# Kernel tuning notes

Hardware: AMD Instinct MI355X
Metric: run time of the kernel (lower is better)

The kernel has to match this reference:

```python
import jax, jax.numpy as jnp
import numpy as np

D_MODEL = 1024
N_HEADS = 16
HEAD_DIM = D_MODEL // N_HEADS
B, S = 2, 2048


def setup_inputs() -> dict:
    key = jax.random.key(0)
    ks = jax.random.split(key, 12)
    std = 1.0 / np.sqrt(D_MODEL)
    mk = lambda k: (jax.random.normal(k, (D_MODEL, D_MODEL), jnp.float32) * std)
    return {
        "query": jax.random.normal(ks[0], (B, S, D_MODEL), jnp.float32),
        "key": jax.random.normal(ks[1], (B, S, D_MODEL), jnp.float32),
        "value": jax.random.normal(ks[2], (B, S, D_MODEL), jnp.float32),
        "Wq": mk(ks[3]), "bq": jnp.zeros((D_MODEL,), jnp.float32),
        "Wk": mk(ks[4]), "bk": jnp.zeros((D_MODEL,), jnp.float32),
        "Wv": mk(ks[5]), "bv": jnp.zeros((D_MODEL,), jnp.float32),
        "Wo": mk(ks[6]), "bo": jnp.zeros((D_MODEL,), jnp.float32),
    }


def reference(query, key, value, Wq, bq, Wk, bk, Wv, bv, Wo, bo):
    b, s, d = query.shape
    # Linear projections (torch Linear: x @ W.T + b)
    q = query @ Wq.T + bq
    k = key @ Wk.T + bk
    v = value @ Wv.T + bv
    # [B, H, S, Dh]
    split = lambda x: x.reshape(b, -1, N_HEADS, HEAD_DIM).transpose(0, 2, 1, 3)
    qh, kh, vh = split(q), split(k), split(v)
    scores = jnp.einsum("bhqd,bhkd->bhqk", qh, kh) / jnp.sqrt(
        jnp.asarray(HEAD_DIM, qh.dtype))
    attn = jax.nn.softmax(scores, axis=-1)
    out = jnp.einsum("bhqk,bhkd->bhqd", attn, vh)
    out = out.transpose(0, 2, 1, 3).reshape(b, -1, N_HEADS * HEAD_DIM)
    return out @ Wo.T + bo
```

## Files before the change

kernel.cpp:

```cpp
#include <hip/hip_runtime.h>
#include <hip/hip_bf16.h>


typedef short bf16x8 __attribute__((ext_vector_type(8)));
typedef short bf16x4 __attribute__((ext_vector_type(4)));
typedef float f32x4  __attribute__((ext_vector_type(4)));

constexpr size_t NE = (size_t)4096 * 1024;
constexpr size_t NW = (size_t)1024 * 1024;

#if __has_builtin(__builtin_amdgcn_exp2f)
#define EXP2(x) __builtin_amdgcn_exp2f(x)
#else
#define EXP2(x) exp2f(x)
#endif

__device__ __forceinline__ short f2bf(float f) {
  __hip_bfloat16 h = __float2bfloat16(f);
  return *reinterpret_cast<short*>(&h);
}

__device__ __forceinline__ void cp16(const short* g, short* l) {
  __builtin_amdgcn_global_load_lds(
      (const __attribute__((address_space(1))) void*)g,
      (__attribute__((address_space(3))) void*)l, 16, 0, 0);
}

__device__ __forceinline__ int xcd_swz(int x, int nblk) {
  return (x & 7) * (nblk >> 3) + (x >> 3);
}

__global__ __launch_bounds__(256) void cvt_kernel(
    const float* q, const float* k, const float* v,
    const float* Wq, const float* Wk, const float* Wv, const float* Wo,
    short* qb, short* kb, short* vb,
    short* Wqb, short* Wkb, short* Wvb, short* Wob) {
  const int y = blockIdx.y;
  const float* s; short* d;
  if (y < 12) {
    const int t = y >> 2;
    const size_t off = (size_t)(y & 3) << 20;
    s = (t == 0 ? q : (t == 1 ? k : v)) + off;
    d = (t == 0 ? qb : (t == 1 ? kb : vb)) + off;
  } else {
    s = (y == 12 ? Wq : (y == 13 ? Wk : (y == 14 ? Wv : Wo)));
    d = (y == 12 ? Wqb : (y == 13 ? Wkb : (y == 14 ? Wvb : Wob)));
  }
  size_t i = (size_t)blockIdx.x * 256 + threadIdx.x;
  float4 val = ((const float4*)s)[i];
  bf16x4 o;
  o[0] = f2bf(val.x); o[1] = f2bf(val.y); o[2] = f2bf(val.z); o[3] = f2bf(val.w);
  ((bf16x4*)d)[i] = o;
}

__global__ __launch_bounds__(256) void gemm_qkv(
    const short* __restrict__ A0, const short* __restrict__ A1, const short* __restrict__ A2,
    const short* __restrict__ W0, const short* __restrict__ W1, const short* __restrict__ W2,
    const float* __restrict__ b0, const float* __restrict__ b1, const float* __restrict__ b2,
    short* __restrict__ C0, short* __restrict__ C1, short* __restrict__ Cv) {
  __shared__ short As[3][128 * 32];
  __shared__ short Bs[3][128 * 32];
  const int which = blockIdx.y;
  const short* A    = which == 0 ? A0 : (which == 1 ? A1 : A2);
  const short* W    = which == 0 ? W0 : (which == 1 ? W1 : W2);
  const float* bias = which == 0 ? b0 : (which == 1 ? b1 : b2);
  const float scale = which == 0 ? 0.18033688011112042f : 1.0f;

  const int tid  = threadIdx.x;
  const int bx   = xcd_swz((int)blockIdx.x, 256);
  const int bm   = bx >> 3;
  const int bn   = bx & 7;
  const int lane = tid & 63, wid = tid >> 6;
  const int g = lane >> 4, l15 = lane & 15;
  const int wm = (wid >> 1) * 64, wn = (wid & 1) * 64;

  const short* Ag = A + (size_t)(bm * 128 + (tid >> 2)) * 1024 + (tid & 3) * 8;
  const short* Wg = W + (size_t)(bn * 128 + (tid >> 2)) * 1024 + (tid & 3) * 8;
  const int wofs = wid * 512;

#define QKV_STAGE(t, b)                               \
  do {                                                \
    const int kk_ = (t) * 32;                         \
    cp16(Ag + kk_,             As[(b)] + wofs);       \
    cp16(Ag + 64 * 1024 + kk_, As[(b)] + wofs + 2048);\
    cp16(Wg + kk_,             Bs[(b)] + wofs);       \
    cp16(Wg + 64 * 1024 + kk_, Bs[(b)] + wofs + 2048);\
  } while (0)

  f32x4 acc[4][4];
#pragma unroll
  for (int i = 0; i < 4; ++i)
#pragma unroll
    for (int j = 0; j < 4; ++j) acc[i][j] = (f32x4){0.f, 0.f, 0.f, 0.f};

  QKV_STAGE(0, 0);
  QKV_STAGE(1, 1);

  for (int t = 0; t < 32; ++t) {
    const int cur = t % 3;
    if (t < 30) {
      QKV_STAGE(t + 2, (t + 2) % 3);
      asm volatile("s_waitcnt vmcnt(8)" ::: "memory");
    } else if (t == 30) {
      asm volatile("s_waitcnt vmcnt(4)" ::: "memory");
    } else {
      asm volatile("s_waitcnt vmcnt(0)" ::: "memory");
    }
    __builtin_amdgcn_s_barrier();

    bf16x8 af[4], bfr[4];
#pragma unroll
    for (int mt = 0; mt < 4; ++mt)
      af[mt] = *(const bf16x8*)&As[cur][(wm + mt * 16 + l15) * 32 + g * 8];
#pragma unroll
    for (int nt = 0; nt < 4; ++nt)
      bfr[nt] = *(const bf16x8*)&Bs[cur][(wn + nt * 16 + l15) * 32 + g * 8];
#pragma unroll
    for (int mt = 0; mt < 4; ++mt)
#pragma unroll
      for (int nt = 0; nt < 4; ++nt)
        acc[mt][nt] = __builtin_amdgcn_mfma_f32_16x16x32_bf16(
            af[mt], bfr[nt], acc[mt][nt], 0, 0, 0);

    asm volatile("s_waitcnt lgkmcnt(0)" ::: "memory");
    __builtin_amdgcn_s_barrier();
  }
#undef QKV_STAGE

  const int col0 = bn * 128 + wn;
  if (which < 2) {
    short* C = which == 0 ? C0 : C1;
#pragma unroll
    for (int nt = 0; nt < 4; ++nt) {
      const int col = col0 + nt * 16 + l15;
      const float bb = bias[col];
#pragma unroll
      for (int mt = 0; mt < 4; ++mt) {
        const int m0 = bm * 128 + wm + mt * 16 + g * 4;
#pragma unroll
        for (int r = 0; r < 4; ++r)
          C[(size_t)(m0 + r) * 1024 + col] = f2bf((acc[mt][nt][r] + bb) * scale);
      }
    }
  } else {
#pragma unroll
    for (int nt = 0; nt < 4; ++nt) {
      const int col = col0 + nt * 16 + l15;
      const int h = col >> 6, dh = col & 63;
      const float bb = bias[col];
#pragma unroll
      for (int mt = 0; mt < 4; ++mt) {
        const int m0 = bm * 128 + wm + mt * 16 + g * 4;
        const int bb_ = m0 >> 11, s0 = m0 & 2047;
        const int k6 = s0 & 63;
        const int cpos = (s0 & ~63) | (((k6 >> 4) & 2) << 4)
                       | (((k6 >> 2) & 3) << 3) | (((k6 >> 4) & 1) << 2);
        bf16x4 o;
#pragma unroll
        for (int r = 0; r < 4; ++r) o[r] = f2bf(acc[mt][nt][r] + bb);
        *(bf16x4*)&Cv[(((size_t)bb_ * 16 + h) * 64 + dh) * 2048 + cpos] = o;
      }
    }
  }
}

__global__ __launch_bounds__(256) void gemm_out(
    const short* __restrict__ A, const short* __restrict__ W,
    const float* __restrict__ bias, float* __restrict__ C) {
  __shared__ short As[3][64 * 32];
  __shared__ short Bs[3][128 * 32];
  const int tid  = threadIdx.x;
  const int bx   = xcd_swz((int)blockIdx.x, 512);
  const int bm   = bx >> 3;
  const int bn   = bx & 7;
  const int lane = tid & 63, wid = tid >> 6;
  const int g = lane >> 4, l15 = lane & 15;
  const int wm = (wid >> 1) * 32, wn = (wid & 1) * 64;

  const short* Ag = A + (size_t)(bm * 64 + (tid >> 2)) * 1024 + (tid & 3) * 8;
  const short* Wg = W + (size_t)(bn * 128 + (tid >> 2)) * 1024 + (tid & 3) * 8;
  const int wofs = wid * 512;

#define OUT_STAGE(t, b)                               \
  do {                                                \
    const int kk_ = (t) * 32;                         \
    cp16(Ag + kk_,             As[(b)] + wofs);       \
    cp16(Wg + kk_,             Bs[(b)] + wofs);       \
    cp16(Wg + 64 * 1024 + kk_, Bs[(b)] + wofs + 2048);\
  } while (0)

  f32x4 acc[2][4];
#pragma unroll
  for (int i = 0; i < 2; ++i)
#pragma unroll
    for (int j = 0; j < 4; ++j) acc[i][j] = (f32x4){0.f, 0.f, 0.f, 0.f};

  OUT_STAGE(0, 0);
  OUT_STAGE(1, 1);

  for (int t = 0; t < 32; ++t) {
    const int cur = t % 3;
    if (t < 30) {
      OUT_STAGE(t + 2, (t + 2) % 3);
      asm volatile("s_waitcnt vmcnt(6)" ::: "memory");
    } else if (t == 30) {
      asm volatile("s_waitcnt vmcnt(3)" ::: "memory");
    } else {
      asm volatile("s_waitcnt vmcnt(0)" ::: "memory");
    }
    __builtin_amdgcn_s_barrier();

    bf16x8 af[2], bfr[4];
#pragma unroll
    for (int mt = 0; mt < 2; ++mt)
      af[mt] = *(const bf16x8*)&As[cur][(wm + mt * 16 + l15) * 32 + g * 8];
#pragma unroll
    for (int nt = 0; nt < 4; ++nt)
      bfr[nt] = *(const bf16x8*)&Bs[cur][(wn + nt * 16 + l15) * 32 + g * 8];
#pragma unroll
    for (int mt = 0; mt < 2; ++mt)
#pragma unroll
      for (int nt = 0; nt < 4; ++nt)
        acc[mt][nt] = __builtin_amdgcn_mfma_f32_16x16x32_bf16(
            af[mt], bfr[nt], acc[mt][nt], 0, 0, 0);

    asm volatile("s_waitcnt lgkmcnt(0)" ::: "memory");
    __builtin_amdgcn_s_barrier();
  }
#undef OUT_STAGE

  const int col0 = bn * 128 + wn;
#pragma unroll
  for (int nt = 0; nt < 4; ++nt) {
    const int col = col0 + nt * 16 + l15;
    const float bb = bias[col];
#pragma unroll
    for (int mt = 0; mt < 2; ++mt) {
      const int m0 = bm * 64 + wm + mt * 16 + g * 4;
#pragma unroll
      for (int r = 0; r < 4; ++r)
        C[(size_t)(m0 + r) * 1024 + col] = acc[mt][nt][r] + bb;
    }
  }
}

__global__ __launch_bounds__(256, 4) void attn_kernel(
    const short* __restrict__ Q, const short* __restrict__ K,
    const short* __restrict__ Vg, short* __restrict__ O) {
  __shared__ __align__(16) short KT[2][64 * 64];
  __shared__ __align__(16) short VT[2][64 * 64];

  const int tid  = threadIdx.x;
  const int bx   = xcd_swz((int)blockIdx.x, 512);
  const int qt   = bx & 15;
  const int bh   = bx >> 4;
  const int b    = bh >> 4, h = bh & 15;
  const int lane = tid & 63, wid = tid >> 6;
  const int g = lane >> 4, l15 = lane & 15;
  const int sx = l15 & 7;

  const int q0 = qt * 128 + wid * 32;
  bf16x8 qf[2][2];
#pragma unroll
  for (int mt = 0; mt < 2; ++mt) {
    const size_t base = (size_t)(b * 2048 + q0 + mt * 16 + l15) * 1024 + h * 64;
    qf[mt][0] = *(const bf16x8*)(Q + base + g * 8);
    qf[mt][1] = *(const bf16x8*)(Q + base + 32 + g * 8);
  }

  f32x4 o_acc[2][4];
#pragma unroll
  for (int i = 0; i < 2; ++i)
#pragma unroll
    for (int j = 0; j < 4; ++j) o_acc[i][j] = (f32x4){0.f, 0.f, 0.f, 0.f};
  float l_i[2] = {0.f, 0.f};

  const int lrow = lane >> 3;
  const int qc   = (lane & 7) ^ lrow;
  const int r0   = wid * 16;
  const short* KgA = K + (size_t)(b * 2048 + r0 + lrow) * 1024 + h * 64 + qc * 8;
  const short* VgA = Vg + (size_t)((b * 16 + h) * 64 + r0 + lrow) * 2048 + qc * 8;

#define ATTN_STAGE(kt_, bf_)                                                 \
  do {                                                                       \
    cp16(KgA + (size_t)(kt_) * 64 * 1024,       &KT[bf_][r0 * 64]);          \
    cp16(KgA + (size_t)((kt_) * 64 + 8) * 1024, &KT[bf_][(r0 + 8) * 64]);    \
    cp16(VgA + (kt_) * 64,                      &VT[bf_][r0 * 64]);          \
    cp16(VgA + (kt_) * 64 + 8 * 2048,           &VT[bf_][(r0 + 8) * 64]);    \
  } while (0)

  ATTN_STAGE(0, 0);

  for (int kt = 0; kt < 32; ++kt) {
    const int cur = kt & 1;
    if (kt < 31) {
      ATTN_STAGE(kt + 1, cur ^ 1);
      asm volatile("s_waitcnt vmcnt(4)" ::: "memory");
    } else {
      asm volatile("s_waitcnt vmcnt(0)" ::: "memory");
    }
    __builtin_amdgcn_s_barrier();

    f32x4 sv[2][4];
#pragma unroll
    for (int nt = 0; nt < 4; ++nt) {
      const int krow = (nt * 16 + l15) * 64;
      bf16x8 kf0 = *(const bf16x8*)&KT[cur][krow + ((g ^ sx) << 3)];
      bf16x8 kf1 = *(const bf16x8*)&KT[cur][krow + (((g + 4) ^ sx) << 3)];
#pragma unroll
      for (int mt = 0; mt < 2; ++mt) {
        f32x4 z = (f32x4){0.f, 0.f, 0.f, 0.f};
        z = __builtin_amdgcn_mfma_f32_16x16x32_bf16(kf0, qf[mt][0], z, 0, 0, 0);
        z = __builtin_amdgcn_mfma_f32_16x16x32_bf16(kf1, qf[mt][1], z, 0, 0, 0);
        sv[mt][nt] = z;
      }
    }

    bf16x8 pf[2][2];
#pragma unroll
    for (int mt = 0; mt < 2; ++mt) {
      float s = 0.f;
#pragma unroll
      for (int nt = 0; nt < 4; ++nt)
#pragma unroll
        for (int r = 0; r < 4; ++r) {
          float p = EXP2(sv[mt][nt][r]);
          s += p;
          pf[mt][nt >> 1][(nt & 1) * 4 + r] = f2bf(p);
        }
      l_i[mt] += s;
    }

#pragma unroll
    for (int nt = 0; nt < 4; ++nt) {
      const int vrow = (nt * 16 + l15) * 64;
      bf16x8 vf0 = *(const bf16x8*)&VT[cur][vrow + ((g ^ sx) << 3)];
      bf16x8 vf1 = *(const bf16x8*)&VT[cur][vrow + (((g + 4) ^ sx) << 3)];
#pragma unroll
      for (int mt = 0; mt < 2; ++mt) {
        o_acc[mt][nt] = __builtin_amdgcn_mfma_f32_16x16x32_bf16(
            vf0, pf[mt][0], o_acc[mt][nt], 0, 0, 0);
        o_acc[mt][nt] = __builtin_amdgcn_mfma_f32_16x16x32_bf16(
            vf1, pf[mt][1], o_acc[mt][nt], 0, 0, 0);
      }
    }

    asm volatile("s_waitcnt lgkmcnt(0)" ::: "memory");
    __builtin_amdgcn_s_barrier();
  }
#undef ATTN_STAGE

#pragma unroll
  for (int mt = 0; mt < 2; ++mt) {
    float l = l_i[mt];
    l += __shfl_xor(l, 16, 64);
    l += __shfl_xor(l, 32, 64);
    const float inv = 1.0f / l;
    const int row = q0 + mt * 16 + l15;
    const size_t base = (size_t)(b * 2048 + row) * 1024 + h * 64;
#pragma unroll
    for (int nt = 0; nt < 4; ++nt) {
      bf16x4 o;
#pragma unroll
      for (int r = 0; r < 4; ++r) o[r] = f2bf(o_acc[mt][nt][r] * inv);
      *(bf16x4*)&O[base + nt * 16 + g * 4] = o;
    }
  }
}

extern "C" void kernel_launch(void* const* d_in, const int* in_sizes, int n_in,
                              void* d_out, int out_size, void* d_ws, size_t ws_size,
                              hipStream_t stream) {
  (void)in_sizes; (void)n_in; (void)out_size; (void)ws_size;
  const float* q  = (const float*)d_in[0];
  const float* k  = (const float*)d_in[1];
  const float* v  = (const float*)d_in[2];
  const float* Wq = (const float*)d_in[3];
  const float* bq = (const float*)d_in[4];
  const float* Wk = (const float*)d_in[5];
  const float* bk = (const float*)d_in[6];
  const float* Wv = (const float*)d_in[7];
  const float* bv = (const float*)d_in[8];
  const float* Wo = (const float*)d_in[9];
  const float* bo = (const float*)d_in[10];
  float* out = (float*)d_out;

  short* qb  = (short*)d_ws;
  short* kb  = qb + NE;
  short* vb  = kb + NE;
  short* Wqb = vb + NE;
  short* Wkb = Wqb + NW;
  short* Wvb = Wkb + NW;
  short* Wob = Wvb + NW;
  short* Qw  = Wob + NW;
  short* Kw  = Qw + NE;
  short* Vtg = Kw + NE;
  short* Ob  = qb;

  cvt_kernel<<<dim3(1024, 16), 256, 0, stream>>>(q, k, v, Wq, Wk, Wv, Wo,
                                                 qb, kb, vb, Wqb, Wkb, Wvb, Wob);
  gemm_qkv<<<dim3(256, 3), 256, 0, stream>>>(qb, kb, vb, Wqb, Wkb, Wvb,
                                             bq, bk, bv, Qw, Kw, Vtg);
  attn_kernel<<<512, 256, 0, stream>>>(Qw, Kw, Vtg, Ob);
  gemm_out<<<512, 256, 0, stream>>>(Ob, Wob, bo, out);
}
```

Before: 208.1 us.

## Swizzle GEMM LDS tiles and halve attention query tile per block

Both GEMM kernels now XOR-swizzle the 16-byte chunk position in each LDS row, applied on the global-to-LDS copy and on the fragment reads, to cut LDS bank conflicts. The attention kernel gives each wave 16 query rows instead of 32, so each block covers 64 queries and the grid doubles to 1024 blocks. That raises parallelism and lowers register use, but every K/V tile is now loaded from global memory and LDS twice as often per query.

Result: slower. 213.9 us (+2.8%).

```diff
diff --git a/kernel.cpp b/kernel.cpp
--- a/kernel.cpp
+++ b/kernel.cpp
@@ -73,9 +73,11 @@
   const int lane = tid & 63, wid = tid >> 6;
   const int g = lane >> 4, l15 = lane & 15;
   const int wm = (wid >> 1) * 64, wn = (wid & 1) * 64;
-
-  const short* Ag = A + (size_t)(bm * 128 + (tid >> 2)) * 1024 + (tid & 3) * 8;
-  const short* Wg = W + (size_t)(bn * 128 + (tid >> 2)) * 1024 + (tid & 3) * 8;
+  const int sk = (l15 >> 1) & 3;
+
+  const int qsw = ((tid & 3) ^ ((tid >> 3) & 3)) * 8;
+  const short* Ag = A + (size_t)(bm * 128 + (tid >> 2)) * 1024 + qsw;
+  const short* Wg = W + (size_t)(bn * 128 + (tid >> 2)) * 1024 + qsw;
   const int wofs = wid * 512;
 
 #define QKV_STAGE(t, b)                               \
@@ -111,10 +113,10 @@
     bf16x8 af[4], bfr[4];
 #pragma unroll
     for (int mt = 0; mt < 4; ++mt)
-      af[mt] = *(const bf16x8*)&As[cur][(wm + mt * 16 + l15) * 32 + g * 8];
+      af[mt] = *(const bf16x8*)&As[cur][(wm + mt * 16 + l15) * 32 + ((g ^ sk)) * 8];
 #pragma unroll
     for (int nt = 0; nt < 4; ++nt)
-      bfr[nt] = *(const bf16x8*)&Bs[cur][(wn + nt * 16 + l15) * 32 + g * 8];
+      bfr[nt] = *(const bf16x8*)&Bs[cur][(wn + nt * 16 + l15) * 32 + ((g ^ sk)) * 8];
 #pragma unroll
     for (int mt = 0; mt < 4; ++mt)
 #pragma unroll
@@ -176,9 +178,11 @@
   const int lane = tid & 63, wid = tid >> 6;
   const int g = lane >> 4, l15 = lane & 15;
   const int wm = (wid >> 1) * 32, wn = (wid & 1) * 64;
-
-  const short* Ag = A + (size_t)(bm * 64 + (tid >> 2)) * 1024 + (tid & 3) * 8;
-  const short* Wg = W + (size_t)(bn * 128 + (tid >> 2)) * 1024 + (tid & 3) * 8;
+  const int sk = (l15 >> 1) & 3;
+
+  const int qsw = ((tid & 3) ^ ((tid >> 3) & 3)) * 8;
+  const short* Ag = A + (size_t)(bm * 64 + (tid >> 2)) * 1024 + qsw;
+  const short* Wg = W + (size_t)(bn * 128 + (tid >> 2)) * 1024 + qsw;
   const int wofs = wid * 512;
 
 #define OUT_STAGE(t, b)                               \
@@ -213,10 +217,10 @@
     bf16x8 af[2], bfr[4];
 #pragma unroll
     for (int mt = 0; mt < 2; ++mt)
-      af[mt] = *(const bf16x8*)&As[cur][(wm + mt * 16 + l15) * 32 + g * 8];
+      af[mt] = *(const bf16x8*)&As[cur][(wm + mt * 16 + l15) * 32 + ((g ^ sk)) * 8];
 #pragma unroll
     for (int nt = 0; nt < 4; ++nt)
-      bfr[nt] = *(const bf16x8*)&Bs[cur][(wn + nt * 16 + l15) * 32 + g * 8];
+      bfr[nt] = *(const bf16x8*)&Bs[cur][(wn + nt * 16 + l15) * 32 + ((g ^ sk)) * 8];
 #pragma unroll
     for (int mt = 0; mt < 2; ++mt)
 #pragma unroll
@@ -251,29 +255,26 @@
   __shared__ __align__(16) short VT[2][64 * 64];
 
   const int tid  = threadIdx.x;
-  const int bx   = xcd_swz((int)blockIdx.x, 512);
-  const int qt   = bx & 15;
-  const int bh   = bx >> 4;
+  const int bx   = xcd_swz((int)blockIdx.x, 1024);
+  const int qt   = bx & 31;
+  const int bh   = bx >> 5;
   const int b    = bh >> 4, h = bh & 15;
   const int lane = tid & 63, wid = tid >> 6;
   const int g = lane >> 4, l15 = lane & 15;
   const int sx = l15 & 7;
 
-  const int q0 = qt * 128 + wid * 32;
-  bf16x8 qf[2][2];
-#pragma unroll
-  for (int mt = 0; mt < 2; ++mt) {
-    const size_t base = (size_t)(b * 2048 + q0 + mt * 16 + l15) * 1024 + h * 64;
-    qf[mt][0] = *(const bf16x8*)(Q + base + g * 8);
-    qf[mt][1] = *(const bf16x8*)(Q + base + 32 + g * 8);
-  }
-
-  f32x4 o_acc[2][4];
-#pragma unroll
-  for (int i = 0; i < 2; ++i)
-#pragma unroll
-    for (int j = 0; j < 4; ++j) o_acc[i][j] = (f32x4){0.f, 0.f, 0.f, 0.f};
-  float l_i[2] = {0.f, 0.f};
+  const int q0 = qt * 64 + wid * 16;
+  bf16x8 qf0, qf1;
+  {
+    const size_t base = (size_t)(b * 2048 + q0 + l15) * 1024 + h * 64;
+    qf0 = *(const bf16x8*)(Q + base + g * 8);
+    qf1 = *(const bf16x8*)(Q + base + 32 + g * 8);
+  }
+
+  f32x4 o_acc[4];
+#pragma unroll
+  for (int j = 0; j < 4; ++j) o_acc[j] = (f32x4){0.f, 0.f, 0.f, 0.f};
+  float l_i = 0.f;
 
   const int lrow = lane >> 3;
   const int qc   = (lane & 7) ^ lrow;
@@ -301,48 +302,39 @@
     }
     __builtin_amdgcn_s_barrier();
 
-    f32x4 sv[2][4];
+    f32x4 sv[4];
 #pragma unroll
     for (int nt = 0; nt < 4; ++nt) {
       const int krow = (nt * 16 + l15) * 64;
       bf16x8 kf0 = *(const bf16x8*)&KT[cur][krow + ((g ^ sx) << 3)];
       bf16x8 kf1 = *(const bf16x8*)&KT[cur][krow + (((g + 4) ^ sx) << 3)];
-#pragma unroll
-      for (int mt = 0; mt < 2; ++mt) {
-        f32x4 z = (f32x4){0.f, 0.f, 0.f, 0.f};
-        z = __builtin_amdgcn_mfma_f32_16x16x32_bf16(kf0, qf[mt][0], z, 0, 0, 0);
-        z = __builtin_amdgcn_mfma_f32_16x16x32_bf16(kf1, qf[mt][1], z, 0, 0, 0);
-        sv[mt][nt] = z;
+      f32x4 z = (f32x4){0.f, 0.f, 0.f, 0.f};
+      z = __builtin_amdgcn_mfma_f32_16x16x32_bf16(kf0, qf0, z, 0, 0, 0);
+      z = __builtin_amdgcn_mfma_f32_16x16x32_bf16(kf1, qf1, z, 0, 0, 0);
+      sv[nt] = z;
+    }
+
+    bf16x8 pf[2];
+    float s = 0.f;
+#pragma unroll
+    for (int nt = 0; nt < 4; ++nt)
+#pragma unroll
+      for (int r = 0; r < 4; ++r) {
+        float p = EXP2(sv[nt][r]);
+        s += p;
+        pf[nt >> 1][(nt & 1) * 4 + r] = f2bf(p);
       }
-    }
-
-    bf16x8 pf[2][2];
-#pragma unroll
-    for (int mt = 0; mt < 2; ++mt) {
-      float s = 0.f;
-#pragma unroll
-      for (int nt = 0; nt < 4; ++nt)
-#pragma unroll
-        for (int r = 0; r < 4; ++r) {
-          float p = EXP2(sv[mt][nt][r]);
-          s += p;
-          pf[mt][nt >> 1][(nt & 1) * 4 + r] = f2bf(p);
-        }
-      l_i[mt] += s;
-    }
+    l_i += s;
 
 #pragma unroll
     for (int nt = 0; nt < 4; ++nt) {
       const int vrow = (nt * 16 + l15) * 64;
       bf16x8 vf0 = *(const bf16x8*)&VT[cur][vrow + ((g ^ sx) << 3)];
       bf16x8 vf1 = *(const bf16x8*)&VT[cur][vrow + (((g + 4) ^ sx) << 3)];
-#pragma unroll
-      for (int mt = 0; mt < 2; ++mt) {
-        o_acc[mt][nt] = __builtin_amdgcn_mfma_f32_16x16x32_bf16(
-            vf0, pf[mt][0], o_acc[mt][nt], 0, 0, 0);
-        o_acc[mt][nt] = __builtin_amdgcn_mfma_f32_16x16x32_bf16(
-            vf1, pf[mt][1], o_acc[mt][nt], 0, 0, 0);
-      }
+      o_acc[nt] = __builtin_amdgcn_mfma_f32_16x16x32_bf16(
+          vf0, pf[0], o_acc[nt], 0, 0, 0);
+      o_acc[nt] = __builtin_amdgcn_mfma_f32_16x16x32_bf16(
+          vf1, pf[1], o_acc[nt], 0, 0, 0);
     }
 
     asm volatile("s_waitcnt lgkmcnt(0)" ::: "memory");
@@ -350,19 +342,18 @@
   }
 #undef ATTN_STAGE
 
-#pragma unroll
-  for (int mt = 0; mt < 2; ++mt) {
-    float l = l_i[mt];
+  {
+    float l = l_i;
     l += __shfl_xor(l, 16, 64);
     l += __shfl_xor(l, 32, 64);
     const float inv = 1.0f / l;
-    const int row = q0 + mt * 16 + l15;
+    const int row = q0 + l15;
     const size_t base = (size_t)(b * 2048 + row) * 1024 + h * 64;
 #pragma unroll
     for (int nt = 0; nt < 4; ++nt) {
       bf16x4 o;
 #pragma unroll
-      for (int r = 0; r < 4; ++r) o[r] = f2bf(o_acc[mt][nt][r] * inv);
+      for (int r = 0; r < 4; ++r) o[r] = f2bf(o_acc[nt][r] * inv);
       *(bf16x4*)&O[base + nt * 16 + g * 4] = o;
     }
   }
@@ -401,6 +392,6 @@
                                                  qb, kb, vb, Wqb, Wkb, Wvb, Wob);
   gemm_qkv<<<dim3(256, 3), 256, 0, stream>>>(qb, kb, vb, Wqb, Wkb, Wvb,
                                              bq, bk, bv, Qw, Kw, Vtg);
-  attn_kernel<<<512, 256, 0, stream>>>(Qw, Kw, Vtg, Ob);
+  attn_kernel<<<1024, 256, 0, stream>>>(Qw, Kw, Vtg, Ob);
   gemm_out<<<512, 256, 0, stream>>>(Ob, Wob, bo, out);
 }
```

## Swizzle GEMM LDS layout and double attention key/value tile per barrier

Applied to the files above, without the earlier changes.

Both projection GEMMs now XOR-swizzle the 16-byte chunk position within each 32-element LDS row, on both the global_load_lds write side and the fragment read side, to cut LDS bank conflicts on the fragment reads. The attention kernel loads two 64-key tiles per pipeline stage and processes them in one barrier interval, which halves the number of barriers and waitcnt syncs. This doubles attention LDS use to 64KB per block, and launch bounds drop to 2 blocks per CU, so fewer waves are resident to hide latency.

Measured after the change: 208.0 us. No clear change (-0.0%).

```diff
diff --git a/kernel.cpp b/kernel.cpp
--- a/kernel.cpp
+++ b/kernel.cpp
@@ -73,9 +73,11 @@
   const int lane = tid & 63, wid = tid >> 6;
   const int g = lane >> 4, l15 = lane & 15;
   const int wm = (wid >> 1) * 64, wn = (wid & 1) * 64;
-
-  const short* Ag = A + (size_t)(bm * 128 + (tid >> 2)) * 1024 + (tid & 3) * 8;
-  const short* Wg = W + (size_t)(bn * 128 + (tid >> 2)) * 1024 + (tid & 3) * 8;
+  const int sk = (l15 >> 1) & 3;
+
+  const int qsw = ((tid & 3) ^ ((tid >> 3) & 3)) * 8;
+  const short* Ag = A + (size_t)(bm * 128 + (tid >> 2)) * 1024 + qsw;
+  const short* Wg = W + (size_t)(bn * 128 + (tid >> 2)) * 1024 + qsw;
   const int wofs = wid * 512;
 
 #define QKV_STAGE(t, b)                               \
@@ -111,10 +113,10 @@
     bf16x8 af[4], bfr[4];
 #pragma unroll
     for (int mt = 0; mt < 4; ++mt)
-      af[mt] = *(const bf16x8*)&As[cur][(wm + mt * 16 + l15) * 32 + g * 8];
+      af[mt] = *(const bf16x8*)&As[cur][(wm + mt * 16 + l15) * 32 + ((g ^ sk)) * 8];
 #pragma unroll
     for (int nt = 0; nt < 4; ++nt)
-      bfr[nt] = *(const bf16x8*)&Bs[cur][(wn + nt * 16 + l15) * 32 + g * 8];
+      bfr[nt] = *(const bf16x8*)&Bs[cur][(wn + nt * 16 + l15) * 32 + ((g ^ sk)) * 8];
 #pragma unroll
     for (int mt = 0; mt < 4; ++mt)
 #pragma unroll
@@ -176,9 +178,11 @@
   const int lane = tid & 63, wid = tid >> 6;
   const int g = lane >> 4, l15 = lane & 15;
   const int wm = (wid >> 1) * 32, wn = (wid & 1) * 64;
-
-  const short* Ag = A + (size_t)(bm * 64 + (tid >> 2)) * 1024 + (tid & 3) * 8;
-  const short* Wg = W + (size_t)(bn * 128 + (tid >> 2)) * 1024 + (tid & 3) * 8;
+  const int sk = (l15 >> 1) & 3;
+
+  const int qsw = ((tid & 3) ^ ((tid >> 3) & 3)) * 8;
+  const short* Ag = A + (size_t)(bm * 64 + (tid >> 2)) * 1024 + qsw;
+  const short* Wg = W + (size_t)(bn * 128 + (tid >> 2)) * 1024 + qsw;
   const int wofs = wid * 512;
 
 #define OUT_STAGE(t, b)                               \
@@ -213,10 +217,10 @@
     bf16x8 af[2], bfr[4];
 #pragma unroll
     for (int mt = 0; mt < 2; ++mt)
-      af[mt] = *(const bf16x8*)&As[cur][(wm + mt * 16 + l15) * 32 + g * 8];
+      af[mt] = *(const bf16x8*)&As[cur][(wm + mt * 16 + l15) * 32 + ((g ^ sk)) * 8];
 #pragma unroll
     for (int nt = 0; nt < 4; ++nt)
-      bfr[nt] = *(const bf16x8*)&Bs[cur][(wn + nt * 16 + l15) * 32 + g * 8];
+      bfr[nt] = *(const bf16x8*)&Bs[cur][(wn + nt * 16 + l15) * 32 + ((g ^ sk)) * 8];
 #pragma unroll
     for (int mt = 0; mt < 2; ++mt)
 #pragma unroll
@@ -244,11 +248,11 @@
   }
 }
 
-__global__ __launch_bounds__(256, 4) void attn_kernel(
+__global__ __launch_bounds__(256, 2) void attn_kernel(
     const short* __restrict__ Q, const short* __restrict__ K,
     const short* __restrict__ Vg, short* __restrict__ O) {
-  __shared__ __align__(16) short KT[2][64 * 64];
-  __shared__ __align__(16) short VT[2][64 * 64];
+  __shared__ __align__(16) short KT[2][2][64 * 64];
+  __shared__ __align__(16) short VT[2][2][64 * 64];
 
   const int tid  = threadIdx.x;
   const int bx   = xcd_swz((int)blockIdx.x, 512);
@@ -281,74 +285,82 @@
   const short* KgA = K + (size_t)(b * 2048 + r0 + lrow) * 1024 + h * 64 + qc * 8;
   const short* VgA = Vg + (size_t)((b * 16 + h) * 64 + r0 + lrow) * 2048 + qc * 8;
 
-#define ATTN_STAGE(kt_, bf_)                                                 \
+#define ATTN_STAGE2(k2_, bf_)                                                \
   do {                                                                       \
-    cp16(KgA + (size_t)(kt_) * 64 * 1024,       &KT[bf_][r0 * 64]);          \
-    cp16(KgA + (size_t)((kt_) * 64 + 8) * 1024, &KT[bf_][(r0 + 8) * 64]);    \
-    cp16(VgA + (kt_) * 64,                      &VT[bf_][r0 * 64]);          \
-    cp16(VgA + (kt_) * 64 + 8 * 2048,           &VT[bf_][(r0 + 8) * 64]);    \
+    const int t0_ = (k2_) * 2, t1_ = t0_ + 1;                                \
+    cp16(KgA + (size_t)t0_ * 64 * 1024,        &KT[bf_][0][r0 * 64]);        \
+    cp16(KgA + (size_t)(t0_ * 64 + 8) * 1024,  &KT[bf_][0][(r0 + 8) * 64]);  \
+    cp16(VgA + t0_ * 64,                       &VT[bf_][0][r0 * 64]);        \
+    cp16(VgA + t0_ * 64 + 8 * 2048,            &VT[bf_][0][(r0 + 8) * 64]);  \
+    cp16(KgA + (size_t)t1_ * 64 * 1024,        &KT[bf_][1][r0 * 64]);        \
+    cp16(KgA + (size_t)(t1_ * 64 + 8) * 1024,  &KT[bf_][1][(r0 + 8) * 64]);  \
+    cp16(VgA + t1_ * 64,                       &VT[bf_][1][r0 * 64]);        \
+    cp16(VgA + t1_ * 64 + 8 * 2048,            &VT[bf_][1][(r0 + 8) * 64]);  \
   } while (0)
 
-  ATTN_STAGE(0, 0);
-
-  for (int kt = 0; kt < 32; ++kt) {
-    const int cur = kt & 1;
-    if (kt < 31) {
-      ATTN_STAGE(kt + 1, cur ^ 1);
-      asm volatile("s_waitcnt vmcnt(4)" ::: "memory");
+  ATTN_STAGE2(0, 0);
+
+  for (int k2 = 0; k2 < 16; ++k2) {
+    const int cur = k2 & 1;
+    if (k2 < 15) {
+      ATTN_STAGE2(k2 + 1, cur ^ 1);
+      asm volatile("s_waitcnt vmcnt(8)" ::: "memory");
     } else {
       asm volatile("s_waitcnt vmcnt(0)" ::: "memory");
     }
     __builtin_amdgcn_s_barrier();
 
-    f32x4 sv[2][4];
-#pragma unroll
-    for (int nt = 0; nt < 4; ++nt) {
-      const int krow = (nt * 16 + l15) * 64;
-      bf16x8 kf0 = *(const bf16x8*)&KT[cur][krow + ((g ^ sx) << 3)];
-      bf16x8 kf1 = *(const bf16x8*)&KT[cur][krow + (((g + 4) ^ sx) << 3)];
+#pragma unroll
+    for (int sub = 0; sub < 2; ++sub) {
+      f32x4 sv[2][4];
+#pragma unroll
+      for (int nt = 0; nt < 4; ++nt) {
+        const int krow = (nt * 16 + l15) * 64;
+        bf16x8 kf0 = *(const bf16x8*)&KT[cur][sub][krow + ((g ^ sx) << 3)];
+        bf16x8 kf1 = *(const bf16x8*)&KT[cur][sub][krow + (((g + 4) ^ sx) << 3)];
+#pragma unroll
+        for (int mt = 0; mt < 2; ++mt) {
+          f32x4 z = (f32x4){0.f, 0.f, 0.f, 0.f};
+          z = __builtin_amdgcn_mfma_f32_16x16x32_bf16(kf0, qf[mt][0], z, 0, 0, 0);
+          z = __builtin_amdgcn_mfma_f32_16x16x32_bf16(kf1, qf[mt][1], z, 0, 0, 0);
+          sv[mt][nt] = z;
+        }
+      }
+
+      bf16x8 pf[2][2];
 #pragma unroll
       for (int mt = 0; mt < 2; ++mt) {
-        f32x4 z = (f32x4){0.f, 0.f, 0.f, 0.f};
-        z = __builtin_amdgcn_mfma_f32_16x16x32_bf16(kf0, qf[mt][0], z, 0, 0, 0);
-        z = __builtin_amdgcn_mfma_f32_16x16x32_bf16(kf1, qf[mt][1], z, 0, 0, 0);
-        sv[mt][nt] = z;
+        float s = 0.f;
+#pragma unroll
+        for (int nt = 0; nt < 4; ++nt)
+#pragma unroll
+          for (int r = 0; r < 4; ++r) {
+            float p = EXP2(sv[mt][nt][r]);
+            s += p;
+            pf[mt][nt >> 1][(nt & 1) * 4 + r] = f2bf(p);
+          }
+        l_i[mt] += s;
       }
-    }
-
-    bf16x8 pf[2][2];
-#pragma unroll
-    for (int mt = 0; mt < 2; ++mt) {
-      float s = 0.f;
-#pragma unroll
-      for (int nt = 0; nt < 4; ++nt)
-#pragma unroll
-        for (int r = 0; r < 4; ++r) {
-          float p = EXP2(sv[mt][nt][r]);
-          s += p;
-          pf[mt][nt >> 1][(nt & 1) * 4 + r] = f2bf(p);
+
+#pragma unroll
+      for (int nt = 0; nt < 4; ++nt) {
+        const int vrow = (nt * 16 + l15) * 64;
+        bf16x8 vf0 = *(const bf16x8*)&VT[cur][sub][vrow + ((g ^ sx) << 3)];
+        bf16x8 vf1 = *(const bf16x8*)&VT[cur][sub][vrow + (((g + 4) ^ sx) << 3)];
+#pragma unroll
+        for (int mt = 0; mt < 2; ++mt) {
+          o_acc[mt][nt] = __builtin_amdgcn_mfma_f32_16x16x32_bf16(
+              vf0, pf[mt][0], o_acc[mt][nt], 0, 0, 0);
+          o_acc[mt][nt] = __builtin_amdgcn_mfma_f32_16x16x32_bf16(
+              vf1, pf[mt][1], o_acc[mt][nt], 0, 0, 0);
         }
-      l_i[mt] += s;
-    }
-
-#pragma unroll
-    for (int nt = 0; nt < 4; ++nt) {
-      const int vrow = (nt * 16 + l15) * 64;
-      bf16x8 vf0 = *(const bf16x8*)&VT[cur][vrow + ((g ^ sx) << 3)];
-      bf16x8 vf1 = *(const bf16x8*)&VT[cur][vrow + (((g + 4) ^ sx) << 3)];
-#pragma unroll
-      for (int mt = 0; mt < 2; ++mt) {
-        o_acc[mt][nt] = __builtin_amdgcn_mfma_f32_16x16x32_bf16(
-            vf0, pf[mt][0], o_acc[mt][nt], 0, 0, 0);
-        o_acc[mt][nt] = __builtin_amdgcn_mfma_f32_16x16x32_bf16(
-            vf1, pf[mt][1], o_acc[mt][nt], 0, 0, 0);
       }
     }
 
     asm volatile("s_waitcnt lgkmcnt(0)" ::: "memory");
     __builtin_amdgcn_s_barrier();
   }
-#undef ATTN_STAGE
+#undef ATTN_STAGE2
 
 #pragma unroll
   for (int mt = 0; mt < 2; ++mt) {
```
